# Performance work log

Hardware: AMD Instinct MI355X
Metric: run time of the kernel (lower is better)

## Reference

```python
import jax, jax.numpy as jnp
import numpy as np

L = 262144
C = 64           # in_channels == out_channels (required by zeros_like scatter)
NUM_MODES = 64

def setup_inputs() -> dict:
    key = jax.random.key(0)
    k1, k2, k3, k4 = jax.random.split(key, 4)
    u = jax.random.normal(k1, (L, C), dtype=jnp.float32)
    y = jax.random.uniform(k2, (1, 1), dtype=jnp.float32)
    scale = 1.0 / (C * C)
    K = scale * jax.random.normal(k3, (2, C, C, NUM_MODES), dtype=jnp.float32)
    # glorot_normal for square (C, C)
    W = jax.random.normal(k4, (C, C), dtype=jnp.float32) * jnp.sqrt(2.0 / (C + C))
    return {"u": u, "y": y, "K": K, "W": W}

def reference(u, y, K, W):
    num_modes = K.shape[-1]
    out_ch = W.shape[0]
    # conditioner: spectral (global) branch
    u_hat = jnp.fft.rfft(u, axis=0)                      # (L//2+1, C) complex64
    Kc = K[0] + 1j * K[1]                                # (C, C, num_modes)
    z_modes = jnp.einsum('xi,iox->xo', u_hat[:num_modes], Kc)  # (num_modes, C)
    z_global = jnp.zeros_like(u_hat).at[:num_modes, :].set(z_modes)
    # conditioner: local branch (gather one spatial row, apply W)
    length = u.shape[0]
    idx = jnp.int32(y * length)[0][0]
    z_local = jnp.dot(W, u[idx, :out_ch])                # (C,)
    # basefield: inverse transform + local shift
    n = 2 * (z_global.shape[0] - 1)                      # == L
    s = jnp.fft.irfft(z_global, n=n, axis=0)             # (L, C)
    return s + z_local
```

## Files before the change

kernel.cpp:

```cpp
#include <hip/hip_runtime.h>

#define LN 262144
#define LMASK 262143
#define NCH 64
#define INV_L (1.0f/262144.0f)

typedef short short8 __attribute__((ext_vector_type(8)));
typedef float f32x4 __attribute__((ext_vector_type(4)));

static __device__ __forceinline__ unsigned short f2bf(float x) {
    union { float f; unsigned u; } v; v.f = x;
    unsigned r = (v.u + 0x7fff + ((v.u >> 16) & 1)) >> 16;
    return (unsigned short)r;
}
static __device__ __forceinline__ float fsin01(float rev) {
    float r; asm("v_sin_f32 %0, %1" : "=v"(r) : "v"(rev)); return r;
}
static __device__ __forceinline__ float fcos01(float rev) {
    float r; asm("v_cos_f32 %0, %1" : "=v"(r) : "v"(rev)); return r;
}

__global__ __launch_bounds__(256) void fno_fwd(const float* __restrict__ u,
                                               float* __restrict__ part, int nb) {
    __shared__ __align__(16) unsigned short Bt[64 * 40];
    const int tid = threadIdx.x;
    const int lane = tid & 63;
    const int w = tid >> 6;
    const int chunk = LN / nb;
    const int ksteps = chunk >> 5;
    const int n0 = blockIdx.x * chunk;

    const int kkst = tid >> 3;
    const int gst = tid & 7;

    const int l15 = lane & 15;
    const int hk = lane >> 4;
    const int m = w * 16 + l15;

    float cR[8], sR[8];
    #pragma unroll
    for (int j = 0; j < 8; ++j) {
        int kk = hk * 8 + j;
        int ph = (m * (n0 + kk)) & LMASK;
        float rev = (float)ph * INV_L;
        cR[j] = fcos01(rev);
        sR[j] = fsin01(rev);
    }
    float cD, sD;
    {
        int ph = (m * 32) & LMASK;
        float rev = (float)ph * INV_L;
        cD = fcos01(rev);
        sD = fsin01(rev);
    }

    f32x4 accC[4], accS[4];
    #pragma unroll
    for (int t = 0; t < 4; ++t) { accC[t] = (f32x4){0,0,0,0}; accS[t] = (f32x4){0,0,0,0}; }

    const float* pg = u + (size_t)(n0 + kkst) * NCH + gst * 8;
    float4 pa = *(const float4*)pg;
    float4 pb = *(const float4*)(pg + 4);

    for (int t = 0; t < ksteps; ++t) {
        __syncthreads();
        {
            float uv[8] = {pa.x, pa.y, pa.z, pa.w, pb.x, pb.y, pb.z, pb.w};
            #pragma unroll
            for (int q = 0; q < 8; ++q)
                Bt[(gst * 8 + q) * 40 + kkst] = f2bf(uv[q]);
        }
        __syncthreads();
        if (t + 1 < ksteps) {
            const float* pn = u + (size_t)(n0 + (t + 1) * 32 + kkst) * NCH + gst * 8;
            pa = *(const float4*)pn;
            pb = *(const float4*)(pn + 4);
        }
        short8 aC, aS;
        #pragma unroll
        for (int j = 0; j < 8; ++j) {
            aC[j] = (short)f2bf(cR[j]);
            aS[j] = (short)f2bf(-sR[j]);
        }
        #pragma unroll
        for (int j = 0; j < 8; ++j) {
            float c2 = cR[j] * cD - sR[j] * sD;
            sR[j] = fmaf(sR[j], cD, cR[j] * sD);
            cR[j] = c2;
        }
        #pragma unroll
        for (int tn = 0; tn < 4; ++tn) {
            const short8 bf = *(const short8*)&Bt[(tn * 16 + l15) * 40 + hk * 8];
            accC[tn] = __builtin_amdgcn_mfma_f32_16x16x32_bf16(aC, bf, accC[tn], 0, 0, 0);
            accS[tn] = __builtin_amdgcn_mfma_f32_16x16x32_bf16(aS, bf, accS[tn], 0, 0, 0);
        }
    }
    float* baseR = part + (size_t)blockIdx.x * 8192;
    #pragma unroll
    for (int tn = 0; tn < 4; ++tn) {
        #pragma unroll
        for (int r = 0; r < 4; ++r) {
            int k = w * 16 + hk * 4 + r;
            int i = tn * 16 + l15;
            baseR[k * 64 + i] = accC[tn][r];
            baseR[4096 + k * 64 + i] = accS[tn][r];
        }
    }
}

__global__ __launch_bounds__(256) void fno_red(const float* __restrict__ part, int nb,
                                               float* __restrict__ uhat) {
    __shared__ float sh[2][128];
    const int tid = threadIdx.x;
    const int j = blockIdx.x * 128 + (tid & 127);
    const int h = tid >> 7;
    float s = 0.f;
    #pragma unroll 8
    for (int b = h; b < nb; b += 2)
        s += part[(size_t)b * 8192 + j];
    sh[h][tid & 127] = s;
    __syncthreads();
    if (h == 0) uhat[j] = sh[0][tid] + sh[1][tid];
}

__global__ __launch_bounds__(64) void fno_coef(const float* __restrict__ uhat,
                                               const float* __restrict__ Kt,
                                               const float* __restrict__ W,
                                               const float* __restrict__ u,
                                               const float* __restrict__ y,
                                               float* __restrict__ coef) {
    const int k = blockIdx.x;
    const int o = threadIdx.x;
    __shared__ float reU[64], imU[64];
    reU[o] = uhat[k * 64 + o];
    imU[o] = uhat[4096 + k * 64 + o];
    __syncthreads();
    float zr = 0.f, zi = 0.f;
    #pragma unroll 8
    for (int ii = 0; ii < 64; ++ii) {
        float k0v = Kt[(size_t)(ii * 64 + o) * 64 + k];
        float k1v = Kt[262144 + (size_t)(ii * 64 + o) * 64 + k];
        zr = fmaf(reU[ii], k0v, fmaf(-imU[ii], k1v, zr));
        zi = fmaf(reU[ii], k1v, fmaf(imU[ii], k0v, zi));
    }
    if (k == 0) {
        const int idx = (int)(y[0] * (float)LN);
        float zl = 0.f;
        for (int ii = 0; ii < 64; ++ii)
            zl = fmaf(W[o * 64 + ii], u[(size_t)idx * 64 + ii], zl);
        coef[o] = zr * INV_L;
        coef[4096 + o] = 0.f;
        coef[8192 + o] = zl;
    } else {
        coef[k * 64 + o] = 2.f * zr * INV_L;
        coef[4096 + k * 64 + o] = -2.f * zi * INV_L;
    }
}

__global__ __launch_bounds__(256) void fno_inv(const float* __restrict__ coef,
                                               float* __restrict__ out) {
    __shared__ __align__(16) unsigned short Bs[64 * 136];
    __shared__ float zloc[64];
    __shared__ float xpose[4][16 * 68];
    const int tid = threadIdx.x;
    const int lane = tid & 63;
    const int w = tid >> 6;

    for (int e = tid; e < 4096; e += 256) {
        int mm = e >> 6, ch = e & 63;
        Bs[ch * 136 + mm] = f2bf(coef[e]);
        Bs[ch * 136 + 64 + mm] = f2bf(coef[4096 + e]);
    }
    if (tid < 64) zloc[tid] = coef[8192 + tid];
    __syncthreads();

    const int l15 = lane & 15;
    const int hk = lane >> 4;
    const int r0 = lane >> 2;
    const int cq = lane & 3;
    float4 zv[4];
    #pragma unroll
    for (int uu = 0; uu < 4; ++uu)
        zv[uu] = *(const float4*)&zloc[cq * 16 + uu * 4];

    for (int p = 0; p < 4; ++p) {
        const int nbase = blockIdx.x * 256 + (p * 4 + w) * 16;
        f32x4 acc[4];
        #pragma unroll
        for (int tn = 0; tn < 4; ++tn) acc[tn] = (f32x4){0,0,0,0};

        const int row = nbase + l15;
        #pragma unroll
        for (int ks = 0; ks < 4; ++ks) {
            const int mbase = ks * 32 + hk * 8 - (ks >= 2 ? 64 : 0);
            short8 af;
            int ph = (row * mbase) & LMASK;
            #pragma unroll
            for (int j = 0; j < 8; ++j) {
                float rev = (float)ph * INV_L;
                float v = (ks < 2) ? fcos01(rev) : fsin01(rev);
                af[j] = (short)f2bf(v);
                ph = (ph + row) & LMASK;
            }
            #pragma unroll
            for (int tn = 0; tn < 4; ++tn) {
                const short8 bf = *(const short8*)&Bs[(tn * 16 + l15) * 136 + ks * 32 + hk * 8];
                acc[tn] = __builtin_amdgcn_mfma_f32_16x16x32_bf16(af, bf, acc[tn], 0, 0, 0);
            }
        }
        #pragma unroll
        for (int tn = 0; tn < 4; ++tn)
            #pragma unroll
            for (int r = 0; r < 4; ++r)
                xpose[w][(hk * 4 + r) * 68 + tn * 16 + l15] = acc[tn][r];
        float* po = out + (size_t)(nbase + r0) * NCH;
        #pragma unroll
        for (int uu = 0; uu < 4; ++uu) {
            float4 v = *(const float4*)&xpose[w][r0 * 68 + cq * 16 + uu * 4];
            v.x += zv[uu].x; v.y += zv[uu].y; v.z += zv[uu].z; v.w += zv[uu].w;
            *(float4*)(po + cq * 16 + uu * 4) = v;
        }
    }
}

extern "C" void kernel_launch(void* const* d_in, const int* in_sizes, int n_in,
                              void* d_out, int out_size, void* d_ws, size_t ws_size,
                              hipStream_t stream) {
    const float* u = (const float*)d_in[0];
    const float* y = (const float*)d_in[1];
    const float* K = (const float*)d_in[2];
    const float* W = (const float*)d_in[3];
    float* out = (float*)d_out;
    float* ws = (float*)d_ws;

    int nb = 512;
    while (nb > 64 && ((size_t)(nb * 8192 + 8192 + 8256) * 4) > ws_size) nb >>= 1;

    float* part = ws;
    float* uhat = ws + (size_t)nb * 8192;
    float* coef = uhat + 8192;

    fno_fwd<<<nb, 256, 0, stream>>>(u, part, nb);
    fno_red<<<64, 256, 0, stream>>>(part, nb, uhat);
    fno_coef<<<64, 64, 0, stream>>>(uhat, K, W, u, y, coef);
    fno_inv<<<1024, 256, 0, stream>>>(coef, out);
}
```

Baseline: 73.49 us.

## Double-buffer forward tiles, fuse reduce with coef, recurrence twiddles in inverse

The forward DFT kernel now double-buffers its bf16 LDS tile and prefetches input two steps ahead, so each step needs one barrier instead of two. The partial-sum reduction and the spectral coefficient kernel are merged into one launch, which drops the intermediate uhat buffer. The inverse kernel builds its twiddle factors by rotation recurrence instead of one sin/cos per element, and the LDS strides and output-store mapping are changed. The recurrence adds rounding drift, and the changed strides may alter bank conflicts.

```diff
diff --git a/kernel.cpp b/kernel.cpp
--- a/kernel.cpp
+++ b/kernel.cpp
@@ -4,6 +4,9 @@
 #define LMASK 262143
 #define NCH 64
 #define INV_L (1.0f/262144.0f)
+#define BSTR 38
+#define ISTR 138
+#define XSTR 66
 
 typedef short short8 __attribute__((ext_vector_type(8)));
 typedef float f32x4 __attribute__((ext_vector_type(4)));
@@ -22,7 +25,7 @@
 
 __global__ __launch_bounds__(256) void fno_fwd(const float* __restrict__ u,
                                                float* __restrict__ part, int nb) {
-    __shared__ __align__(16) unsigned short Bt[64 * 40];
+    __shared__ __align__(16) unsigned short Bt[2][64 * BSTR];
     const int tid = threadIdx.x;
     const int lane = tid & 63;
     const int w = tid >> 6;
@@ -40,41 +43,52 @@
     float cR[8], sR[8];
     #pragma unroll
     for (int j = 0; j < 8; ++j) {
-        int kk = hk * 8 + j;
-        int ph = (m * (n0 + kk)) & LMASK;
-        float rev = (float)ph * INV_L;
-        cR[j] = fcos01(rev);
-        sR[j] = fsin01(rev);
+        int ph = (m * (n0 + hk * 8 + j)) & LMASK;
+        cR[j] = fcos01((float)ph * INV_L);
+        sR[j] = fsin01((float)ph * INV_L);
     }
     float cD, sD;
     {
         int ph = (m * 32) & LMASK;
-        float rev = (float)ph * INV_L;
-        cD = fcos01(rev);
-        sD = fsin01(rev);
+        cD = fcos01((float)ph * INV_L);
+        sD = fsin01((float)ph * INV_L);
     }
 
     f32x4 accC[4], accS[4];
     #pragma unroll
     for (int t = 0; t < 4; ++t) { accC[t] = (f32x4){0,0,0,0}; accS[t] = (f32x4){0,0,0,0}; }
 
-    const float* pg = u + (size_t)(n0 + kkst) * NCH + gst * 8;
-    float4 pa = *(const float4*)pg;
-    float4 pb = *(const float4*)(pg + 4);
+    const float* __restrict__ ub = u + (size_t)(n0 + kkst) * NCH + gst * 8;
+    const size_t tstep = 32 * NCH;
+
+    float4 a0 = *(const float4*)(ub);
+    float4 a1 = *(const float4*)(ub + 4);
+    float4 b0 = *(const float4*)(ub + tstep);
+    float4 b1 = *(const float4*)(ub + tstep + 4);
+    {
+        float uv[8] = {a0.x, a0.y, a0.z, a0.w, a1.x, a1.y, a1.z, a1.w};
+        #pragma unroll
+        for (int q = 0; q < 8; ++q)
+            Bt[0][(gst * 8 + q) * BSTR + kkst] = f2bf(uv[q]);
+    }
+    a0 = b0; a1 = b1;
+    b0 = *(const float4*)(ub + 2 * tstep);
+    b1 = *(const float4*)(ub + 2 * tstep + 4);
 
     for (int t = 0; t < ksteps; ++t) {
         __syncthreads();
-        {
-            float uv[8] = {pa.x, pa.y, pa.z, pa.w, pb.x, pb.y, pb.z, pb.w};
+        if (t + 1 < ksteps) {
+            float uv[8] = {a0.x, a0.y, a0.z, a0.w, a1.x, a1.y, a1.z, a1.w};
+            unsigned short* bt = Bt[(t + 1) & 1];
             #pragma unroll
             for (int q = 0; q < 8; ++q)
-                Bt[(gst * 8 + q) * 40 + kkst] = f2bf(uv[q]);
-        }
-        __syncthreads();
-        if (t + 1 < ksteps) {
-            const float* pn = u + (size_t)(n0 + (t + 1) * 32 + kkst) * NCH + gst * 8;
-            pa = *(const float4*)pn;
-            pb = *(const float4*)(pn + 4);
+                bt[(gst * 8 + q) * BSTR + kkst] = f2bf(uv[q]);
+        }
+        a0 = b0; a1 = b1;
+        if (t + 3 < ksteps) {
+            const float* pn = ub + (size_t)(t + 3) * tstep;
+            b0 = *(const float4*)(pn);
+            b1 = *(const float4*)(pn + 4);
         }
         short8 aC, aS;
         #pragma unroll
@@ -88,9 +102,10 @@
             sR[j] = fmaf(sR[j], cD, cR[j] * sD);
             cR[j] = c2;
         }
+        const unsigned short* bt = Bt[t & 1];
         #pragma unroll
         for (int tn = 0; tn < 4; ++tn) {
-            const short8 bf = *(const short8*)&Bt[(tn * 16 + l15) * 40 + hk * 8];
+            const short8 bf = *(const short8*)&bt[(tn * 16 + l15) * BSTR + hk * 8];
             accC[tn] = __builtin_amdgcn_mfma_f32_16x16x32_bf16(aC, bf, accC[tn], 0, 0, 0);
             accS[tn] = __builtin_amdgcn_mfma_f32_16x16x32_bf16(aS, bf, accS[tn], 0, 0, 0);
         }
@@ -108,117 +123,124 @@
     }
 }
 
-__global__ __launch_bounds__(256) void fno_red(const float* __restrict__ part, int nb,
-                                               float* __restrict__ uhat) {
-    __shared__ float sh[2][128];
-    const int tid = threadIdx.x;
-    const int j = blockIdx.x * 128 + (tid & 127);
-    const int h = tid >> 7;
+__global__ __launch_bounds__(512) void fno_redcoef(const float* __restrict__ part, int nb,
+                                                   const float* __restrict__ Kt,
+                                                   const float* __restrict__ W,
+                                                   const float* __restrict__ u,
+                                                   const float* __restrict__ y,
+                                                   float* __restrict__ coef) {
+    const int k = blockIdx.x;
+    const int t = threadIdx.x;
+    const int j = t & 127;
+    const int h = t >> 7;
+
+    const float* __restrict__ pb = part + (size_t)k * 64 + (j & 63) + ((j >> 6) ? 4096 : 0);
     float s = 0.f;
     #pragma unroll 8
-    for (int b = h; b < nb; b += 2)
-        s += part[(size_t)b * 8192 + j];
-    sh[h][tid & 127] = s;
+    for (int b = h; b < nb; b += 4)
+        s += pb[(size_t)b * 8192];
+
+    __shared__ float red[4][128];
+    __shared__ float uh[128];
+    red[h][j] = s;
     __syncthreads();
-    if (h == 0) uhat[j] = sh[0][tid] + sh[1][tid];
-}
-
-__global__ __launch_bounds__(64) void fno_coef(const float* __restrict__ uhat,
-                                               const float* __restrict__ Kt,
-                                               const float* __restrict__ W,
-                                               const float* __restrict__ u,
-                                               const float* __restrict__ y,
-                                               float* __restrict__ coef) {
-    const int k = blockIdx.x;
-    const int o = threadIdx.x;
-    __shared__ float reU[64], imU[64];
-    reU[o] = uhat[k * 64 + o];
-    imU[o] = uhat[4096 + k * 64 + o];
+    if (t < 128) uh[t] = red[0][t] + red[1][t] + red[2][t] + red[3][t];
     __syncthreads();
-    float zr = 0.f, zi = 0.f;
-    #pragma unroll 8
-    for (int ii = 0; ii < 64; ++ii) {
-        float k0v = Kt[(size_t)(ii * 64 + o) * 64 + k];
-        float k1v = Kt[262144 + (size_t)(ii * 64 + o) * 64 + k];
-        zr = fmaf(reU[ii], k0v, fmaf(-imU[ii], k1v, zr));
-        zi = fmaf(reU[ii], k1v, fmaf(imU[ii], k0v, zi));
-    }
-    if (k == 0) {
-        const int idx = (int)(y[0] * (float)LN);
-        float zl = 0.f;
-        for (int ii = 0; ii < 64; ++ii)
-            zl = fmaf(W[o * 64 + ii], u[(size_t)idx * 64 + ii], zl);
-        coef[o] = zr * INV_L;
-        coef[4096 + o] = 0.f;
-        coef[8192 + o] = zl;
-    } else {
-        coef[k * 64 + o] = 2.f * zr * INV_L;
-        coef[4096 + k * 64 + o] = -2.f * zi * INV_L;
+
+    if (t < 64) {
+        const int o = t;
+        float zr = 0.f, zi = 0.f;
+        #pragma unroll 8
+        for (int ii = 0; ii < 64; ++ii) {
+            float k0v = Kt[(size_t)(ii * 64 + o) * 64 + k];
+            float k1v = Kt[262144 + (size_t)(ii * 64 + o) * 64 + k];
+            zr = fmaf(uh[ii], k0v, fmaf(-uh[64 + ii], k1v, zr));
+            zi = fmaf(uh[ii], k1v, fmaf(uh[64 + ii], k0v, zi));
+        }
+        if (k == 0) {
+            const int idx = (int)(y[0] * (float)LN);
+            float zl = 0.f;
+            for (int ii = 0; ii < 64; ++ii)
+                zl = fmaf(W[o * 64 + ii], u[(size_t)idx * 64 + ii], zl);
+            coef[o] = zr * INV_L;
+            coef[4096 + o] = 0.f;
+            coef[8192 + o] = zl;
+        } else {
+            coef[k * 64 + o] = 2.f * zr * INV_L;
+            coef[4096 + k * 64 + o] = -2.f * zi * INV_L;
+        }
     }
 }
 
 __global__ __launch_bounds__(256) void fno_inv(const float* __restrict__ coef,
                                                float* __restrict__ out) {
-    __shared__ __align__(16) unsigned short Bs[64 * 136];
+    __shared__ __align__(16) unsigned short Bs[64 * ISTR];
     __shared__ float zloc[64];
-    __shared__ float xpose[4][16 * 68];
+    __shared__ float xpose[4][16 * XSTR];
     const int tid = threadIdx.x;
     const int lane = tid & 63;
     const int w = tid >> 6;
 
     for (int e = tid; e < 4096; e += 256) {
         int mm = e >> 6, ch = e & 63;
-        Bs[ch * 136 + mm] = f2bf(coef[e]);
-        Bs[ch * 136 + 64 + mm] = f2bf(coef[4096 + e]);
+        Bs[ch * ISTR + mm] = f2bf(coef[e]);
+        Bs[ch * ISTR + 64 + mm] = f2bf(coef[4096 + e]);
     }
     if (tid < 64) zloc[tid] = coef[8192 + tid];
     __syncthreads();
 
     const int l15 = lane & 15;
     const int hk = lane >> 4;
-    const int r0 = lane >> 2;
-    const int cq = lane & 3;
-    float4 zv[4];
-    #pragma unroll
-    for (int uu = 0; uu < 4; ++uu)
-        zv[uu] = *(const float4*)&zloc[cq * 16 + uu * 4];
+    const int rl = lane >> 4;
+    const int cq = lane & 15;
+    float4 zv = *(const float4*)&zloc[cq * 4];
 
     for (int p = 0; p < 4; ++p) {
         const int nbase = blockIdx.x * 256 + (p * 4 + w) * 16;
+        const int row = nbase + l15;
+        float cstp = fcos01((float)row * INV_L);
+        float sstp = fsin01((float)row * INV_L);
+
+        short8 aF[4];
+        #pragma unroll
+        for (int h = 0; h < 2; ++h) {
+            const int m0 = h * 32 + hk * 8;
+            const int ph = (row * m0) & LMASK;
+            float c = fcos01((float)ph * INV_L);
+            float s = fsin01((float)ph * INV_L);
+            #pragma unroll
+            for (int jj = 0; jj < 8; ++jj) {
+                aF[h][jj] = (short)f2bf(c);
+                aF[2 + h][jj] = (short)f2bf(s);
+                float c2 = c * cstp - s * sstp;
+                s = fmaf(s, cstp, c * sstp);
+                c = c2;
+            }
+        }
+
         f32x4 acc[4];
         #pragma unroll
         for (int tn = 0; tn < 4; ++tn) acc[tn] = (f32x4){0,0,0,0};
-
-        const int row = nbase + l15;
         #pragma unroll
         for (int ks = 0; ks < 4; ++ks) {
-            const int mbase = ks * 32 + hk * 8 - (ks >= 2 ? 64 : 0);
-            short8 af;
-            int ph = (row * mbase) & LMASK;
-            #pragma unroll
-            for (int j = 0; j < 8; ++j) {
-                float rev = (float)ph * INV_L;
-                float v = (ks < 2) ? fcos01(rev) : fsin01(rev);
-                af[j] = (short)f2bf(v);
-                ph = (ph + row) & LMASK;
+            #pragma unroll
+            for (int tn = 0; tn < 4; ++tn) {
+                const short8 bf = *(const short8*)&Bs[(tn * 16 + l15) * ISTR + ks * 32 + hk * 8];
+                acc[tn] = __builtin_amdgcn_mfma_f32_16x16x32_bf16(aF[ks], bf, acc[tn], 0, 0, 0);
             }
-            #pragma unroll
-            for (int tn = 0; tn < 4; ++tn) {
-                const short8 bf = *(const short8*)&Bs[(tn * 16 + l15) * 136 + ks * 32 + hk * 8];
-                acc[tn] = __builtin_amdgcn_mfma_f32_16x16x32_bf16(af, bf, acc[tn], 0, 0, 0);
-            }
         }
         #pragma unroll
         for (int tn = 0; tn < 4; ++tn)
             #pragma unroll
             for (int r = 0; r < 4; ++r)
-                xpose[w][(hk * 4 + r) * 68 + tn * 16 + l15] = acc[tn][r];
-        float* po = out + (size_t)(nbase + r0) * NCH;
-        #pragma unroll
-        for (int uu = 0; uu < 4; ++uu) {
-            float4 v = *(const float4*)&xpose[w][r0 * 68 + cq * 16 + uu * 4];
-            v.x += zv[uu].x; v.y += zv[uu].y; v.z += zv[uu].z; v.w += zv[uu].w;
-            *(float4*)(po + cq * 16 + uu * 4) = v;
+                xpose[w][(hk * 4 + r) * XSTR + tn * 16 + l15] = acc[tn][r];
+        __builtin_amdgcn_s_waitcnt(0);
+        #pragma unroll
+        for (int rg = 0; rg < 4; ++rg) {
+            const int rowl = rg * 4 + rl;
+            float4 v = *(const float4*)&xpose[w][rowl * XSTR + cq * 4];
+            v.x += zv.x; v.y += zv.y; v.z += zv.z; v.w += zv.w;
+            *(float4*)(out + (size_t)(nbase + rowl) * NCH + cq * 4) = v;
         }
     }
 }
@@ -234,14 +256,12 @@
     float* ws = (float*)d_ws;
 
     int nb = 512;
-    while (nb > 64 && ((size_t)(nb * 8192 + 8192 + 8256) * 4) > ws_size) nb >>= 1;
+    while (nb > 64 && ((size_t)(nb * 8192 + 8256) * 4) > ws_size) nb >>= 1;
 
     float* part = ws;
-    float* uhat = ws + (size_t)nb * 8192;
-    float* coef = uhat + 8192;
+    float* coef = ws + (size_t)nb * 8192;
 
     fno_fwd<<<nb, 256, 0, stream>>>(u, part, nb);
-    fno_red<<<64, 256, 0, stream>>>(part, nb, uhat);
-    fno_coef<<<64, 64, 0, stream>>>(uhat, K, W, u, y, coef);
+    fno_redcoef<<<64, 512, 0, stream>>>(part, nb, K, W, u, y, coef);
     fno_inv<<<1024, 256, 0, stream>>>(coef, out);
 }
```

Result: faster. 64.72 us (-11.9%).
